# Kernel optimization log

Hardware: AMD Instinct MI355X
Metric: run time of the kernel (lower is better)

## Reference

```python
import jax, jax.numpy as jnp
import numpy as np

N_NODES = 100000
N_EDGES = 1600000
D = 64        # in_channels == edge_dim == out_channels
HID = 128     # GIN_MLP hidden_dim
EPS = 0.0


def setup_inputs() -> dict:
    key = jax.random.key(0)
    ks = jax.random.split(key, 10)
    x = jax.random.normal(ks[0], (N_NODES, D), dtype=jnp.float32)
    edge_index = jax.random.randint(ks[1], (2, N_EDGES), 0, N_NODES, dtype=jnp.int64)
    edge_attr = jax.random.normal(ks[2], (N_EDGES, D), dtype=jnp.float32)
    s = 1.0 / np.sqrt(D)
    sh = 1.0 / np.sqrt(HID)
    # GINEConv internal edge projection: Linear(edge_dim, in_channels)
    lin_w = jax.random.uniform(ks[3], (D, D), jnp.float32, -s, s)
    lin_b = jax.random.uniform(ks[4], (D,), jnp.float32, -s, s)
    # GIN_MLP: Linear(in, hidden) -> ReLU -> Linear(hidden, out)
    w0 = jax.random.uniform(ks[5], (HID, D), jnp.float32, -s, s)
    b0 = jax.random.uniform(ks[6], (HID,), jnp.float32, -s, s)
    w1 = jax.random.uniform(ks[7], (D, HID), jnp.float32, -sh, sh)
    b1 = jax.random.uniform(ks[8], (D,), jnp.float32, -sh, sh)
    return {"x": x, "edge_index": edge_index, "edge_attr": edge_attr,
            "lin_w": lin_w, "lin_b": lin_b, "w0": w0, "b0": b0, "w1": w1, "b1": b1}


def reference(x, edge_index, edge_attr, lin_w, lin_b, w0, b0, w1, b1):
    src, dst = edge_index[0], edge_index[1]
    # project edge features to node dim, add gathered source features, relu
    e = edge_attr @ lin_w.T + lin_b                  # [E, D]
    msg = jax.nn.relu(x[src] + e)                    # [E, D]
    # scatter-sum into destination nodes
    agg = jax.ops.segment_sum(msg, dst, num_segments=N_NODES)  # [N, D]
    h = (1.0 + EPS) * x + agg                        # [N, D]
    # 2-layer MLP
    h = jax.nn.relu(h @ w0.T + b0)                   # [N, HID]
    return h @ w1.T + b1                             # [N, D]
```

## Files before the change

kernel.cpp:

```cpp
#include <hip/hip_runtime.h>
#include <hip/hip_bf16.h>

#define NN 100000
#define NE 1600000
#define DD 64
#define HID 128

__global__ __launch_bounds__(256, 4)
void edge_kernel(const float* __restrict__ edge_attr,
                 const int*   __restrict__ edge_index,
                 const float* __restrict__ x,
                 const float* __restrict__ lin_w,
                 const float* __restrict__ lin_b,
                 float* agg)
{
    const int lane = threadIdx.x & 63;
    int wid = blockIdx.x * (blockDim.x >> 6) + (threadIdx.x >> 6);
    wid = __builtin_amdgcn_readfirstlane(wid);
    const int nwaves = gridDim.x * (blockDim.x >> 6);

    float w[DD];
    const float4* wrow = reinterpret_cast<const float4*>(lin_w + lane * DD);
    #pragma unroll
    for (int q = 0; q < DD / 4; ++q) {
        float4 v = wrow[q];
        w[4 * q + 0] = v.x; w[4 * q + 1] = v.y;
        w[4 * q + 2] = v.z; w[4 * q + 3] = v.w;
    }
    #pragma unroll
    for (int k = 0; k < DD; ++k) asm volatile("" : "+v"(w[k]));
    const float bj = lin_b[lane];

    for (int e = wid; e < NE; e += nwaves) {
        const int src = edge_index[e];
        const int dst = edge_index[NE + e];
        const float* ea = edge_attr + (size_t)e * DD;

        float xv = x[(size_t)src * DD + lane];

        float a0 = 0.f, a1 = 0.f, a2 = 0.f, a3 = 0.f;
        #pragma unroll
        for (int k = 0; k < DD; k += 4) {
            a0 = fmaf(ea[k + 0], w[k + 0], a0);
            a1 = fmaf(ea[k + 1], w[k + 1], a1);
            a2 = fmaf(ea[k + 2], w[k + 2], a2);
            a3 = fmaf(ea[k + 3], w[k + 3], a3);
        }
        float m = xv + bj + ((a0 + a1) + (a2 + a3));
        m = m > 0.0f ? m : 0.0f;
        unsafeAtomicAdd(&agg[(size_t)dst * DD + lane], m);
    }
}

__global__ __launch_bounds__(256, 2)
void mlp_kernel(const float* __restrict__ h_in,
                float* out,
                const float* __restrict__ w0, const float* __restrict__ b0,
                const float* __restrict__ w1, const float* __restrict__ b1)
{
    __shared__ float W1t[HID * DD];
    __shared__ float h1buf[4][2][HID];

    for (int i = threadIdx.x; i < HID * DD; i += blockDim.x) {
        int j = i >> 7;
        int k = i & 127;
        W1t[k * DD + j] = w1[i];
    }
    __syncthreads();

    const int lane = threadIdx.x & 63;
    const int wv   = threadIdx.x >> 6;
    int wid = blockIdx.x * (blockDim.x >> 6) + wv;
    wid = __builtin_amdgcn_readfirstlane(wid);
    const int nwaves = gridDim.x * (blockDim.x >> 6);

    float w0a[DD], w0b[DD];
    const float4* r0 = reinterpret_cast<const float4*>(w0 + lane * DD);
    const float4* r1 = reinterpret_cast<const float4*>(w0 + (lane + 64) * DD);
    #pragma unroll
    for (int q = 0; q < DD / 4; ++q) {
        float4 va = r0[q], vb = r1[q];
        w0a[4*q+0]=va.x; w0a[4*q+1]=va.y; w0a[4*q+2]=va.z; w0a[4*q+3]=va.w;
        w0b[4*q+0]=vb.x; w0b[4*q+1]=vb.y; w0b[4*q+2]=vb.z; w0b[4*q+3]=vb.w;
    }
    #pragma unroll
    for (int k = 0; k < DD; ++k) {
        asm volatile("" : "+v"(w0a[k]));
        asm volatile("" : "+v"(w0b[k]));
    }
    const float b0a = b0[lane], b0b = b0[lane + 64];
    const float b1j = b1[lane];

    const int npairs = NN / 2;
    for (int p = wid; p < npairs; p += nwaves) {
        #pragma unroll
        for (int t = 0; t < 2; ++t) {
            const float* h = h_in + (size_t)(2 * p + t) * DD;
            float a0 = b0a, a1 = b0b, c0 = 0.f, c1 = 0.f;
            #pragma unroll
            for (int k = 0; k < DD; k += 2) {
                float hk0 = h[k], hk1 = h[k + 1];
                a0 = fmaf(hk0, w0a[k], a0);
                a1 = fmaf(hk0, w0b[k], a1);
                c0 = fmaf(hk1, w0a[k + 1], c0);
                c1 = fmaf(hk1, w0b[k + 1], c1);
            }
            a0 += c0; a1 += c1;
            a0 = a0 > 0.0f ? a0 : 0.0f;
            a1 = a1 > 0.0f ? a1 : 0.0f;
            h1buf[wv][t][lane]      = a0;
            h1buf[wv][t][lane + 64] = a1;
        }

        const float4* h0v = reinterpret_cast<const float4*>(&h1buf[wv][0][0]);
        const float4* h1v = reinterpret_cast<const float4*>(&h1buf[wv][1][0]);
        float acc0 = b1j, acc1 = b1j;
        #pragma unroll
        for (int k4 = 0; k4 < HID / 4; ++k4) {
            float4 p0 = h0v[k4];
            float4 p1 = h1v[k4];
            int kb = 4 * k4;
            float wk0 = W1t[(kb + 0) * DD + lane];
            float wk1 = W1t[(kb + 1) * DD + lane];
            float wk2 = W1t[(kb + 2) * DD + lane];
            float wk3 = W1t[(kb + 3) * DD + lane];
            acc0 = fmaf(p0.x, wk0, acc0); acc1 = fmaf(p1.x, wk0, acc1);
            acc0 = fmaf(p0.y, wk1, acc0); acc1 = fmaf(p1.y, wk1, acc1);
            acc0 = fmaf(p0.z, wk2, acc0); acc1 = fmaf(p1.z, wk2, acc1);
            acc0 = fmaf(p0.w, wk3, acc0); acc1 = fmaf(p1.w, wk3, acc1);
        }
        out[(size_t)(2 * p + 0) * DD + lane] = acc0;
        out[(size_t)(2 * p + 1) * DD + lane] = acc1;
    }
}

extern "C" void kernel_launch(void* const* d_in, const int* in_sizes, int n_in,
                              void* d_out, int out_size, void* d_ws, size_t ws_size,
                              hipStream_t stream) {
    const float* x         = (const float*)d_in[0];
    const int*   edge_index= (const int*)  d_in[1];
    const float* edge_attr = (const float*)d_in[2];
    const float* lin_w     = (const float*)d_in[3];
    const float* lin_b     = (const float*)d_in[4];
    const float* w0        = (const float*)d_in[5];
    const float* b0        = (const float*)d_in[6];
    const float* w1        = (const float*)d_in[7];
    const float* b1        = (const float*)d_in[8];
    float* out = (float*)d_out;

    const size_t hbytes = (size_t)NN * DD * sizeof(float);
    float* hbuf = (ws_size >= hbytes) ? (float*)d_ws : out;

    hipMemcpyAsync(hbuf, x, hbytes, hipMemcpyDeviceToDevice, stream);

    edge_kernel<<<2048, 256, 0, stream>>>(edge_attr, edge_index, x,
                                          lin_w, lin_b, hbuf);
    mlp_kernel<<<1024, 256, 0, stream>>>(hbuf, out, w0, b0, w1, b1);
}
```

Measured before the change: 1.413 ms.

## Stage edge_attr tiles into LDS with async loads and tile the MLP

The edge kernel now streams 64-edge tiles of edge_attr into double-buffered shared memory with global_load_lds, prefetching the next tile while the current one is processed. This replaces the per-lane scalar-broadcast global reads of each edge row with vectorized LDS reads. The MLP kernel is restructured so each block loads 64 node rows into LDS, then computes both layers in phases, reloading weight rows into registers per phase and keeping the hidden activations in LDS. The new layout adds block-level barriers per tile and uses more shared memory, which may reduce occupancy.

```diff
diff --git a/kernel.cpp b/kernel.cpp
--- a/kernel.cpp
+++ b/kernel.cpp
@@ -1,10 +1,30 @@
 #include <hip/hip_runtime.h>
-#include <hip/hip_bf16.h>
 
 #define NN 100000
 #define NE 1600000
 #define DD 64
 #define HID 128
+
+typedef const __attribute__((address_space(1))) unsigned int* gas1_t;
+typedef __attribute__((address_space(3)))       unsigned int* las3_t;
+
+__device__ __forceinline__ void pin64(float (&w)[DD]) {
+    #pragma unroll
+    for (int k = 0; k < DD; k += 8)
+        asm volatile("" : "+v"(w[k+0]), "+v"(w[k+1]), "+v"(w[k+2]), "+v"(w[k+3]),
+                          "+v"(w[k+4]), "+v"(w[k+5]), "+v"(w[k+6]), "+v"(w[k+7]));
+}
+
+__device__ __forceinline__ void load_row64(float (&w)[DD], const float* __restrict__ src) {
+    const float4* s4 = reinterpret_cast<const float4*>(src);
+    #pragma unroll
+    for (int q = 0; q < DD / 4; ++q) {
+        float4 v = s4[q];
+        w[4*q+0] = v.x; w[4*q+1] = v.y; w[4*q+2] = v.z; w[4*q+3] = v.w;
+    }
+}
+
+#define ETILE 64
 
 __global__ __launch_bounds__(256, 4)
 void edge_kernel(const float* __restrict__ edge_attr,
@@ -14,138 +34,188 @@
                  const float* __restrict__ lin_b,
                  float* agg)
 {
+    __shared__ float ea[2][ETILE * DD];
+
     const int lane = threadIdx.x & 63;
-    int wid = blockIdx.x * (blockDim.x >> 6) + (threadIdx.x >> 6);
-    wid = __builtin_amdgcn_readfirstlane(wid);
-    const int nwaves = gridDim.x * (blockDim.x >> 6);
+    const int wvu  = __builtin_amdgcn_readfirstlane(threadIdx.x >> 6);
 
     float w[DD];
-    const float4* wrow = reinterpret_cast<const float4*>(lin_w + lane * DD);
-    #pragma unroll
-    for (int q = 0; q < DD / 4; ++q) {
-        float4 v = wrow[q];
-        w[4 * q + 0] = v.x; w[4 * q + 1] = v.y;
-        w[4 * q + 2] = v.z; w[4 * q + 3] = v.w;
-    }
-    #pragma unroll
-    for (int k = 0; k < DD; ++k) asm volatile("" : "+v"(w[k]));
+    load_row64(w, lin_w + lane * DD);
     const float bj = lin_b[lane];
 
-    for (int e = wid; e < NE; e += nwaves) {
-        const int src = edge_index[e];
-        const int dst = edge_index[NE + e];
-        const float* ea = edge_attr + (size_t)e * DD;
-
-        float xv = x[(size_t)src * DD + lane];
-
-        float a0 = 0.f, a1 = 0.f, a2 = 0.f, a3 = 0.f;
-        #pragma unroll
-        for (int k = 0; k < DD; k += 4) {
-            a0 = fmaf(ea[k + 0], w[k + 0], a0);
-            a1 = fmaf(ea[k + 1], w[k + 1], a1);
-            a2 = fmaf(ea[k + 2], w[k + 2], a2);
-            a3 = fmaf(ea[k + 3], w[k + 3], a3);
-        }
-        float m = xv + bj + ((a0 + a1) + (a2 + a3));
-        m = m > 0.0f ? m : 0.0f;
-        unsafeAtomicAdd(&agg[(size_t)dst * DD + lane], m);
-    }
-}
-
-__global__ __launch_bounds__(256, 2)
+    const int ntiles = NE / ETILE;
+    const int tstep  = gridDim.x;
+    int t = blockIdx.x;
+
+    {
+        const float* g = edge_attr + (size_t)t * (ETILE * DD);
+        #pragma unroll
+        for (int c = 0; c < 4; ++c) {
+            const int off = c * 1024 + wvu * 256;
+            __builtin_amdgcn_global_load_lds((gas1_t)(g + off + lane * 4),
+                                             (las3_t)(&ea[0][off]), 16, 0, 0);
+        }
+    }
+    __syncthreads();
+
+    int cur = 0;
+    for (; t < ntiles; t += tstep) {
+        const int tn = t + tstep;
+        if (tn < ntiles) {
+            const float* g = edge_attr + (size_t)tn * (ETILE * DD);
+            #pragma unroll
+            for (int c = 0; c < 4; ++c) {
+                const int off = c * 1024 + wvu * 256;
+                __builtin_amdgcn_global_load_lds((gas1_t)(g + off + lane * 4),
+                                                 (las3_t)(&ea[cur ^ 1][off]), 16, 0, 0);
+            }
+        }
+
+        pin64(w);
+
+        const int ebase = t * ETILE + wvu * 16;
+        for (int i = 0; i < 16; ++i) {
+            const int eg  = ebase + i;
+            const int src = edge_index[eg];
+            const int dst = edge_index[NE + eg];
+            float xv = x[(size_t)src * DD + lane];
+
+            const float4* ev =
+                reinterpret_cast<const float4*>(&ea[cur][(wvu * 16 + i) * DD]);
+            float a0 = 0.f, a1 = 0.f, a2 = 0.f, a3 = 0.f;
+            #pragma unroll
+            for (int q = 0; q < 16; ++q) {
+                float4 e4 = ev[q];
+                a0 = fmaf(e4.x, w[4*q+0], a0);
+                a1 = fmaf(e4.y, w[4*q+1], a1);
+                a2 = fmaf(e4.z, w[4*q+2], a2);
+                a3 = fmaf(e4.w, w[4*q+3], a3);
+            }
+            float m = xv + bj + ((a0 + a1) + (a2 + a3));
+            m = m > 0.0f ? m : 0.0f;
+            unsafeAtomicAdd(&agg[(size_t)dst * DD + lane], m);
+        }
+        __syncthreads();
+        cur ^= 1;
+    }
+}
+
+#define MT 64
+
+__global__ __launch_bounds__(256, 3)
 void mlp_kernel(const float* __restrict__ h_in,
-                float* out,
+                float* __restrict__ out,
                 const float* __restrict__ w0, const float* __restrict__ b0,
                 const float* __restrict__ w1, const float* __restrict__ b1)
 {
-    __shared__ float W1t[HID * DD];
-    __shared__ float h1buf[4][2][HID];
-
-    for (int i = threadIdx.x; i < HID * DD; i += blockDim.x) {
-        int j = i >> 7;
-        int k = i & 127;
-        W1t[k * DD + j] = w1[i];
+    __shared__ float hls[MT * DD];
+    __shared__ float h1s[MT * HID];
+
+    const int lane = threadIdx.x & 63;
+    const int wvu  = __builtin_amdgcn_readfirstlane(threadIdx.x >> 6);
+    const int nb   = blockIdx.x * MT;
+
+    const float b0a = b0[lane], b0b = b0[lane + 64], b1j = b1[lane];
+
+    #pragma unroll
+    for (int c = 0; c < 4; ++c) {
+        const int off = c * 1024 + wvu * 256;
+        if (nb * DD + off + lane * 4 < NN * DD)
+            __builtin_amdgcn_global_load_lds((gas1_t)(h_in + (size_t)nb * DD + off + lane * 4),
+                                             (las3_t)(&hls[off]), 16, 0, 0);
     }
     __syncthreads();
 
-    const int lane = threadIdx.x & 63;
-    const int wv   = threadIdx.x >> 6;
-    int wid = blockIdx.x * (blockDim.x >> 6) + wv;
-    wid = __builtin_amdgcn_readfirstlane(wid);
-    const int nwaves = gridDim.x * (blockDim.x >> 6);
-
-    float w0a[DD], w0b[DD];
-    const float4* r0 = reinterpret_cast<const float4*>(w0 + lane * DD);
-    const float4* r1 = reinterpret_cast<const float4*>(w0 + (lane + 64) * DD);
-    #pragma unroll
-    for (int q = 0; q < DD / 4; ++q) {
-        float4 va = r0[q], vb = r1[q];
-        w0a[4*q+0]=va.x; w0a[4*q+1]=va.y; w0a[4*q+2]=va.z; w0a[4*q+3]=va.w;
-        w0b[4*q+0]=vb.x; w0b[4*q+1]=vb.y; w0b[4*q+2]=vb.z; w0b[4*q+3]=vb.w;
-    }
-    #pragma unroll
-    for (int k = 0; k < DD; ++k) {
-        asm volatile("" : "+v"(w0a[k]));
-        asm volatile("" : "+v"(w0b[k]));
-    }
-    const float b0a = b0[lane], b0b = b0[lane + 64];
-    const float b1j = b1[lane];
-
-    const int npairs = NN / 2;
-    for (int p = wid; p < npairs; p += nwaves) {
-        #pragma unroll
-        for (int t = 0; t < 2; ++t) {
-            const float* h = h_in + (size_t)(2 * p + t) * DD;
-            float a0 = b0a, a1 = b0b, c0 = 0.f, c1 = 0.f;
-            #pragma unroll
-            for (int k = 0; k < DD; k += 2) {
-                float hk0 = h[k], hk1 = h[k + 1];
-                a0 = fmaf(hk0, w0a[k], a0);
-                a1 = fmaf(hk0, w0b[k], a1);
-                c0 = fmaf(hk1, w0a[k + 1], c0);
-                c1 = fmaf(hk1, w0b[k + 1], c1);
-            }
-            a0 += c0; a1 += c1;
-            a0 = a0 > 0.0f ? a0 : 0.0f;
-            a1 = a1 > 0.0f ? a1 : 0.0f;
-            h1buf[wv][t][lane]      = a0;
-            h1buf[wv][t][lane + 64] = a1;
-        }
-
-        const float4* h0v = reinterpret_cast<const float4*>(&h1buf[wv][0][0]);
-        const float4* h1v = reinterpret_cast<const float4*>(&h1buf[wv][1][0]);
-        float acc0 = b1j, acc1 = b1j;
-        #pragma unroll
-        for (int k4 = 0; k4 < HID / 4; ++k4) {
-            float4 p0 = h0v[k4];
-            float4 p1 = h1v[k4];
-            int kb = 4 * k4;
-            float wk0 = W1t[(kb + 0) * DD + lane];
-            float wk1 = W1t[(kb + 1) * DD + lane];
-            float wk2 = W1t[(kb + 2) * DD + lane];
-            float wk3 = W1t[(kb + 3) * DD + lane];
-            acc0 = fmaf(p0.x, wk0, acc0); acc1 = fmaf(p1.x, wk0, acc1);
-            acc0 = fmaf(p0.y, wk1, acc0); acc1 = fmaf(p1.y, wk1, acc1);
-            acc0 = fmaf(p0.z, wk2, acc0); acc1 = fmaf(p1.z, wk2, acc1);
-            acc0 = fmaf(p0.w, wk3, acc0); acc1 = fmaf(p1.w, wk3, acc1);
-        }
-        out[(size_t)(2 * p + 0) * DD + lane] = acc0;
-        out[(size_t)(2 * p + 1) * DD + lane] = acc1;
+    float w[DD];
+    float acc2[16];
+
+    load_row64(w, w0 + lane * DD);
+    pin64(w);
+    for (int nl = 0; nl < 16; ++nl) {
+        const int node = wvu * 16 + nl;
+        const float4* hv = reinterpret_cast<const float4*>(&hls[node * DD]);
+        float a0 = b0a, a1 = 0.f, a2 = 0.f, a3 = 0.f;
+        #pragma unroll
+        for (int q = 0; q < 16; ++q) {
+            float4 h4 = hv[q];
+            a0 = fmaf(h4.x, w[4*q+0], a0);
+            a1 = fmaf(h4.y, w[4*q+1], a1);
+            a2 = fmaf(h4.z, w[4*q+2], a2);
+            a3 = fmaf(h4.w, w[4*q+3], a3);
+        }
+        float v = (a0 + a1) + (a2 + a3);
+        h1s[node * HID + lane] = v > 0.0f ? v : 0.0f;
+    }
+
+    load_row64(w, w0 + (lane + 64) * DD);
+    pin64(w);
+    for (int nl = 0; nl < 16; ++nl) {
+        const int node = wvu * 16 + nl;
+        const float4* hv = reinterpret_cast<const float4*>(&hls[node * DD]);
+        float a0 = b0b, a1 = 0.f, a2 = 0.f, a3 = 0.f;
+        #pragma unroll
+        for (int q = 0; q < 16; ++q) {
+            float4 h4 = hv[q];
+            a0 = fmaf(h4.x, w[4*q+0], a0);
+            a1 = fmaf(h4.y, w[4*q+1], a1);
+            a2 = fmaf(h4.z, w[4*q+2], a2);
+            a3 = fmaf(h4.w, w[4*q+3], a3);
+        }
+        float v = (a0 + a1) + (a2 + a3);
+        h1s[node * HID + 64 + lane] = v > 0.0f ? v : 0.0f;
+    }
+
+    load_row64(w, w1 + lane * HID);
+    pin64(w);
+    #pragma unroll
+    for (int nl = 0; nl < 16; ++nl) {
+        const int node = wvu * 16 + nl;
+        const float4* pv = reinterpret_cast<const float4*>(&h1s[node * HID]);
+        float a0 = b1j, a1 = 0.f, a2 = 0.f, a3 = 0.f;
+        #pragma unroll
+        for (int q = 0; q < 16; ++q) {
+            float4 p4 = pv[q];
+            a0 = fmaf(p4.x, w[4*q+0], a0);
+            a1 = fmaf(p4.y, w[4*q+1], a1);
+            a2 = fmaf(p4.z, w[4*q+2], a2);
+            a3 = fmaf(p4.w, w[4*q+3], a3);
+        }
+        acc2[nl] = (a0 + a1) + (a2 + a3);
+    }
+
+    load_row64(w, w1 + lane * HID + 64);
+    pin64(w);
+    #pragma unroll
+    for (int nl = 0; nl < 16; ++nl) {
+        const int node = wvu * 16 + nl;
+        const float4* pv = reinterpret_cast<const float4*>(&h1s[node * HID + 64]);
+        float a0 = 0.f, a1 = 0.f, a2 = 0.f, a3 = 0.f;
+        #pragma unroll
+        for (int q = 0; q < 16; ++q) {
+            float4 p4 = pv[q];
+            a0 = fmaf(p4.x, w[4*q+0], a0);
+            a1 = fmaf(p4.y, w[4*q+1], a1);
+            a2 = fmaf(p4.z, w[4*q+2], a2);
+            a3 = fmaf(p4.w, w[4*q+3], a3);
+        }
+        const int gn = nb + node;
+        if (gn < NN)
+            out[(size_t)gn * DD + lane] = acc2[nl] + ((a0 + a1) + (a2 + a3));
     }
 }
 
 extern "C" void kernel_launch(void* const* d_in, const int* in_sizes, int n_in,
                               void* d_out, int out_size, void* d_ws, size_t ws_size,
                               hipStream_t stream) {
-    const float* x         = (const float*)d_in[0];
-    const int*   edge_index= (const int*)  d_in[1];
-    const float* edge_attr = (const float*)d_in[2];
-    const float* lin_w     = (const float*)d_in[3];
-    const float* lin_b     = (const float*)d_in[4];
-    const float* w0        = (const float*)d_in[5];
-    const float* b0        = (const float*)d_in[6];
-    const float* w1        = (const float*)d_in[7];
-    const float* b1        = (const float*)d_in[8];
+    const float* x          = (const float*)d_in[0];
+    const int*   edge_index = (const int*)  d_in[1];
+    const float* edge_attr  = (const float*)d_in[2];
+    const float* lin_w      = (const float*)d_in[3];
+    const float* lin_b      = (const float*)d_in[4];
+    const float* w0         = (const float*)d_in[5];
+    const float* b0         = (const float*)d_in[6];
+    const float* w1         = (const float*)d_in[7];
+    const float* b1         = (const float*)d_in[8];
     float* out = (float*)d_out;
 
     const size_t hbytes = (size_t)NN * DD * sizeof(float);
@@ -155,5 +225,5 @@
 
     edge_kernel<<<2048, 256, 0, stream>>>(edge_attr, edge_index, x,
                                           lin_w, lin_b, hbuf);
-    mlp_kernel<<<1024, 256, 0, stream>>>(hbuf, out, w0, b0, w1, b1);
-}
+    mlp_kernel<<<(NN + MT - 1) / MT, 256, 0, stream>>>(hbuf, out, w0, b0, w1, b1);
+}
```

Measured after the change: 1.848 ms. +30.8%, slower.
